# Optimization experiments

Hardware: AMD Instinct MI355X
Metric: run time of the kernel (lower is better)

The kernel has to match this reference:

```python
import jax, jax.numpy as jnp
import numpy as np

FS = 250; WIN = 250; STRIDE = 50; NC = 5; DM = 128; NH = 4; NL = 3; C = 62; L = 2000
BANDS = [(1, 4), (4, 8), (8, 12), (12, 16), (16, 20), (20, 30), (30, 45)]
UPDATE_RATE = 0.2
SIZES = np.array([13, 13, 12, 12, 12])  # channels//NC with remainder spread (62 = 2*13 + 3*12)
EPS = 1e-9


def _cdist(a, b):
    # Euclidean pairwise distance over last dim; ... batch dims broadcast.
    d2 = (a * a).sum(-1)[..., :, None] + (b * b).sum(-1)[..., None, :] \
         - 2.0 * jnp.einsum('...id,...jd->...ij', a, b)
    return jnp.sqrt(jnp.maximum(d2, 0.0))


def _extract_features(x):
    # PSDDEFeatureExtractor: sliding windows, hann, rfft, band power, DE, per-(b,c) normalization.
    b, c, l = x.shape
    nw = (l - WIN) // STRIDE + 1
    idx = np.arange(nw)[:, None] * STRIDE + np.arange(WIN)[None, :]
    win = x[:, :, idx]
    hann = 0.5 * (1.0 - jnp.cos(2.0 * jnp.pi * jnp.arange(WIN, dtype=x.dtype) / WIN))
    win = win * hann
    ps = jnp.abs(jnp.fft.rfft(win, n=WIN, axis=-1)) ** 2 / WIN  # (b,c,nw,126)
    psd = jnp.stack([ps[..., lo:hi].mean(-1) for lo, hi in BANDS], axis=-1)  # (b,c,nw,7)
    de = 0.5 * jnp.log(2.0 * jnp.pi * jnp.e * psd + EPS)
    def norm(f):
        m = f.mean((-2, -1), keepdims=True)
        s = f.std((-2, -1), keepdims=True, ddof=1)  # torch.std is unbiased
        return (f - m) / (s + EPS)
    return jnp.concatenate([norm(psd), norm(de)], axis=-1)     # (b,c,nw,14)


def _fps(dist, k):
    # Batched farthest-point sampling on (b,c,c) distance matrices -> (b,k) indices.
    take = lambda i: jnp.take_along_axis(dist, i[:, None, None], axis=1)[:, 0]  # (b,c)
    start = jnp.argmax(dist.sum(-1), axis=-1)                  # (b,)
    def step(md, _):
        far = jnp.argmax(md, axis=-1)
        return jnp.minimum(md, take(far)), far
    _, rest = jax.lax.scan(step, take(start), None, length=k - 1)
    return jnp.concatenate([start[:, None], rest.T], axis=1)


def _cluster_assignments(features, pos_emb):
    # ClusterManager.forward on fresh buffers (initialize -> temp centers -> EMA -> capacity assign).
    features = jax.lax.stop_gradient(features)
    pos_emb = jax.lax.stop_gradient(pos_emb)
    b, c = features.shape[:2]
    pos = pos_emb[0]                                           # (c,3)
    centers = pos[_fps(_cdist(pos, pos)[None], NC)[0]]         # (NC,3) FPS init
    # per-sample farthest channels on flattened features
    ff = features.reshape(b, c, -1)
    temp_idx = _fps(_cdist(ff, ff), NC)                        # (b,NC)
    center_coords = jnp.take_along_axis(pos_emb, temp_idx[:, :, None], axis=1)  # (b,NC,3)
    temp_assign = jnp.argmin(_cdist(pos_emb, center_coords), axis=-1)           # (b,c)
    flat_a = temp_assign.reshape(-1)
    flat_p = pos_emb.reshape(-1, 3)
    sums = jax.ops.segment_sum(flat_p, flat_a, num_segments=NC)
    cnts = jax.ops.segment_sum(jnp.ones((b * c,), flat_p.dtype), flat_a, num_segments=NC)
    avg = jnp.where(cnts[:, None] > 0, sums / jnp.maximum(cnts, 1.0)[:, None], 0.0)  # (NC,3)
    matching = jnp.argmin(_cdist(centers, avg), axis=1)
    centers = (1.0 - UPDATE_RATE) * centers + UPDATE_RATE * avg[matching]
    # capacity-constrained greedy assignment (sequential over channels)
    sizes = jnp.asarray(SIZES)
    order = jnp.argsort(_cdist(pos, centers), axis=1)          # (c,NC) preference order
    def step(counts, cand):
        avail = counts[cand] < sizes[cand]
        cl = cand[jnp.argmax(avail)]
        return counts.at[cl].add(1), cl
    _, assign = jax.lax.scan(step, jnp.zeros((NC,), jnp.int32), order)
    return assign                                              # (c,)


def _ln(x, g, b):
    m = x.mean(-1, keepdims=True)
    v = x.var(-1, keepdims=True)
    return (x - m) / jnp.sqrt(v + 1e-5) * g + b


def _mha(h, wqkv, bq, wo, bo_):
    b, t, d = h.shape
    dh = d // NH
    qkv = h @ wqkv.T + bq
    q, k, v = jnp.split(qkv, 3, axis=-1)
    sp = lambda z: z.reshape(b, t, NH, dh).transpose(0, 2, 1, 3)  # bhtd
    q, k, v = sp(q), sp(k), sp(v)
    att = jax.nn.softmax(jnp.einsum('bhqd,bhkd->bhqk', q, k) / jnp.sqrt(jnp.float32(dh)), axis=-1)
    o = jnp.einsum('bhqk,bhkd->bhqd', att, v).transpose(0, 2, 1, 3).reshape(b, t, d)
    return o @ wo.T + bo_


def _forward(x, pos_emb, proj_w, proj_b, proj_ln_g, proj_ln_b, pos_enc,
             Wqkv, bqkv, Wo, bo, W1, b1, W2, b2, ln1_g, ln1_b, ln2_g, ln2_b):
    b = x.shape[0]
    feats = _extract_features(x)                               # (b,C,36,14)
    pf = feats.reshape(b, C, -1) @ proj_w.T + proj_b
    pf = jax.nn.relu(_ln(pf, proj_ln_g, proj_ln_b))            # (b,C,DM)
    assign = _cluster_assignments(feats, pos_emb)              # (C,)
    # per-cluster mean of projected channel features (counts == SIZES by capacity constraint)
    sums = jax.ops.segment_sum(pf.swapaxes(0, 1), assign, num_segments=NC)  # (NC,b,DM)
    tokens = (sums / jnp.asarray(SIZES, pf.dtype)[:, None, None]).swapaxes(0, 1)  # (b,NC,DM)
    h = tokens + pos_enc
    for i in range(NL):  # post-norm TransformerEncoderLayer, eval mode (dropout=0)
        h = _ln(h + _mha(h, Wqkv[i], bqkv[i], Wo[i], bo[i]), ln1_g[i], ln1_b[i])
        ff = jax.nn.relu(h @ W1[i].T + b1[i]) @ W2[i].T + b2[i]
        h = _ln(h + ff, ln2_g[i], ln2_b[i])
    return h                                                   # (b,NC,DM)


def setup_inputs() -> dict:
    key = jax.random.key(0)
    ks = jax.random.split(key, 16)
    d_flat = 36 * 14  # n_windows * (7 psd + 7 de)
    s = 0.05
    return {
        'x': jax.random.normal(ks[0], (128, C, L), jnp.float32),
        'pos_emb': jax.random.normal(ks[1], (128, C, 3), jnp.float32),
        'proj_w': jax.random.normal(ks[2], (DM, d_flat), jnp.float32) * s,
        'proj_b': jax.random.normal(ks[3], (DM,), jnp.float32) * s,
        'proj_ln_g': jnp.ones((DM,), jnp.float32),
        'proj_ln_b': jnp.zeros((DM,), jnp.float32),
        'pos_enc': jax.random.normal(ks[4], (1, NC, DM), jnp.float32),
        'Wqkv': jax.random.normal(ks[5], (NL, 3 * DM, DM), jnp.float32) * s,
        'bqkv': jax.random.normal(ks[6], (NL, 3 * DM), jnp.float32) * s,
        'Wo': jax.random.normal(ks[7], (NL, DM, DM), jnp.float32) * s,
        'bo': jax.random.normal(ks[8], (NL, DM), jnp.float32) * s,
        'W1': jax.random.normal(ks[9], (NL, 2 * DM, DM), jnp.float32) * s,
        'b1': jax.random.normal(ks[10], (NL, 2 * DM), jnp.float32) * s,
        'W2': jax.random.normal(ks[11], (NL, DM, 2 * DM), jnp.float32) * s,
        'b2': jax.random.normal(ks[12], (NL, DM), jnp.float32) * s,
        'ln1_g': jnp.ones((NL, DM), jnp.float32),
        'ln1_b': jnp.zeros((NL, DM), jnp.float32),
        'ln2_g': jnp.ones((NL, DM), jnp.float32),
        'ln2_b': jnp.zeros((NL, DM), jnp.float32),
    }


def reference(x, pos_emb, proj_w, proj_b, proj_ln_g, proj_ln_b, pos_enc,
              Wqkv, bqkv, Wo, bo, W1, b1, W2, b2, ln1_g, ln1_b, ln2_g, ln2_b):
    return _forward(x, pos_emb, proj_w, proj_b, proj_ln_g, proj_ln_b, pos_enc,
                    Wqkv, bqkv, Wo, bo, W1, b1, W2, b2, ln1_g, ln1_b, ln2_g, ln2_b)
```

## Files before the change

### kernel.cpp

```cpp
#include <hip/hip_runtime.h>
#include <hip/hip_bf16.h>


typedef unsigned int u32;

#define N_SIG   7936
#define FDIM    504
#define DM      128

__device__ __constant__ int   bstart_c[7] = {1,4,8,12,16,20,30};
__device__ __constant__ int   bcnt_c[7]   = {3,4,4,4,4,10,15};
__device__ __constant__ float bandcnt_c[7] = {3.f,4.f,4.f,4.f,4.f,10.f,15.f};

__device__ __constant__ float twr_c[5] = {
    1.0f, 0.30901699437494745f, -0.8090169943749475f,
    -0.8090169943749475f, 0.30901699437494745f};
__device__ __constant__ float twi_c[5] = {
    0.0f, -0.9510565162951535f, -0.5877852522924731f,
    0.5877852522924731f, 0.9510565162951535f};

static __device__ __forceinline__ void bred2(float& a, float& b, volatile float* scr, int tid){
    #pragma unroll
    for (int off = 32; off > 0; off >>= 1){
        a += __shfl_down(a, off, 64);
        b += __shfl_down(b, off, 64);
    }
    if ((tid & 63) == 0){ scr[tid>>6] = a; scr[2 + (tid>>6)] = b; }
    __syncthreads();
    a = scr[0] + scr[1];
    b = scr[2] + scr[3];
    __syncthreads();
}

static __device__ __forceinline__ void bred2h(float& a, float& b, volatile float* scr, int tid){
    #pragma unroll
    for (int off = 32; off > 0; off >>= 1){
        a += __shfl_down(a, off, 64);
        b += __shfl_down(b, off, 64);
    }
    if (tid < 128 && (tid & 63) == 0){ scr[tid>>6] = a; scr[2 + (tid>>6)] = b; }
    __syncthreads();
    a = scr[0] + scr[1];
    b = scr[2] + scr[3];
    __syncthreads();
}

static __device__ __forceinline__ float2 combine5(const float* __restrict__ Cb,
                                                  int w, int kk){
    const int k5 = kk % 5;
    const float* cb = Cb + ((size_t)(w*46 + kk))*2;
    float ar = 0.f, ai = 0.f;
    int m = 0;
    #pragma unroll
    for (int c = 0; c < 5; ++c){
        float2 cv = *(const float2*)(cb + c*92);
        float tr = twr_c[m], ti = twi_c[m];
        ar = fmaf(tr, cv.x, ar); ar = fmaf(-ti, cv.y, ar);
        ai = fmaf(tr, cv.y, ai); ai = fmaf(ti, cv.x, ai);
        m += k5; if (m >= 5) m -= 5;
    }
    float2 o; o.x = ar; o.y = ai;
    return o;
}

__global__ __launch_bounds__(256) void basis_kernel(float* __restrict__ basis)
{
    int idx = blockIdx.x*256 + threadIdx.x;
    if (idx >= 1150) return;
    int kp = idx / 50;
    int n  = idx - kp*50;
    const float TPO = 0.025132741228718345f;
    int k0 = 2*kp, k1 = 2*kp + 1;
    float s0, c0, s1, c1;
    sincosf((float)((k0*n) % 250) * TPO, &s0, &c0);
    sincosf((float)((k1*n) % 250) * TPO, &s1, &c1);
    float4 v; v.x = c0; v.y = -s0; v.z = c1; v.w = -s1;
    ((float4*)basis)[idx] = v;
}

__global__ __launch_bounds__(256) void feat_kernel(
        const float* __restrict__ x, const float* __restrict__ basis,
        float* __restrict__ feats)
{
    __shared__ __align__(16) float xs[2000];
    __shared__ __align__(16) float Cb[3680];
    __shared__ float scr[16];

    const int tid = threadIdx.x;
    const int sig = blockIdx.x;

    {
        const float4* xg = (const float4*)(x + (size_t)sig*2000);
        for (int i = tid; i < 500; i += 256) ((float4*)xs)[i] = xg[i];
    }
    __syncthreads();

    for (int item = tid; item < 920; item += 256){
        const int kp = item / 40;
        const int j  = item - kp*40;
        const float2* xp = (const float2*)(xs + 50*j);
        const float4* bp = ((const float4*)basis) + kp*50;
        float cr0=0.f, ci0=0.f, cr1=0.f, ci1=0.f;
        #pragma unroll 5
        for (int t = 0; t < 25; ++t){
            float2 xv = xp[t];
            float4 b0 = bp[2*t], b1 = bp[2*t+1];
            cr0 = fmaf(xv.x, b0.x, cr0); ci0 = fmaf(xv.x, b0.y, ci0);
            cr1 = fmaf(xv.x, b0.z, cr1); ci1 = fmaf(xv.x, b0.w, ci1);
            cr0 = fmaf(xv.y, b1.x, cr0); ci0 = fmaf(xv.y, b1.y, ci0);
            cr1 = fmaf(xv.y, b1.z, cr1); ci1 = fmaf(xv.y, b1.w, ci1);
        }
        float4 o; o.x = cr0; o.y = ci0; o.z = cr1; o.w = ci1;
        *(float4*)(Cb + ((size_t)(j*46 + 2*kp))*2) = o;
    }
    __syncthreads();

    {
        const int i0 = tid, i1 = tid + 256, i2 = tid + 512, i3 = tid + 768;
        float2 r0, r1, r2, r3;
        { int w = 18 + i0/46, k = i0 - (i0/46)*46; r0 = combine5(Cb, w, k); }
        { int w = 18 + i1/46, k = i1 - (i1/46)*46; r1 = combine5(Cb, w, k); }
        { int w = 18 + i2/46, k = i2 - (i2/46)*46; r2 = combine5(Cb, w, k); }
        if (i3 < 828){ int w = 18 + i3/46, k = i3 - (i3/46)*46; r3 = combine5(Cb, w, k); }
        __syncthreads();
        { int w = 18 + i0/46, k = i0 - (i0/46)*46; *(float2*)(Cb + (w+4)*92 + 2*k) = r0; }
        { int w = 18 + i1/46, k = i1 - (i1/46)*46; *(float2*)(Cb + (w+4)*92 + 2*k) = r1; }
        { int w = 18 + i2/46, k = i2 - (i2/46)*46; *(float2*)(Cb + (w+4)*92 + 2*k) = r2; }
        if (i3 < 828){ int w = 18 + i3/46, k = i3 - (i3/46)*46; *(float2*)(Cb + (w+4)*92 + 2*k) = r3; }
    }
    __syncthreads();

    {
        const int i0 = tid, i1 = tid + 256, i2 = tid + 512, i3 = tid + 768;
        float2 r0, r1, r2, r3;
        { int w = i0/46, k = i0 - (i0/46)*46; r0 = combine5(Cb, w, k); }
        { int w = i1/46, k = i1 - (i1/46)*46; r1 = combine5(Cb, w, k); }
        { int w = i2/46, k = i2 - (i2/46)*46; r2 = combine5(Cb, w, k); }
        if (i3 < 828){ int w = i3/46, k = i3 - (i3/46)*46; r3 = combine5(Cb, w, k); }
        __syncthreads();
        { int w = i0/46, k = i0 - (i0/46)*46; *(float2*)(Cb + w*92 + 2*k) = r0; }
        { int w = i1/46, k = i1 - (i1/46)*46; *(float2*)(Cb + w*92 + 2*k) = r1; }
        { int w = i2/46, k = i2 - (i2/46)*46; *(float2*)(Cb + w*92 + 2*k) = r2; }
        if (i3 < 828){ int w = i3/46, k = i3 - (i3/46)*46; *(float2*)(Cb + w*92 + 2*k) = r3; }
    }
    __syncthreads();

    float psd = 0.f, de = 0.f;
    float s1p = 0.f, s2p = 0.f, s1d = 0.f, s2d = 0.f;
    int w = 0, bi = 0;
    if (tid < 252){
        w  = tid / 7;
        bi = tid - w*7;
        const int st = bstart_c[bi], cn = bcnt_c[bi];
        const float2* Xrow = (const float2*)(Cb + ((w < 18) ? w*92 : (w+4)*92));
        float2 xm = Xrow[st-1], xc = Xrow[st];
        float p = 0.f;
        for (int q = 0; q < cn; ++q){
            float2 xp = Xrow[st+q+1];
            float Hr = 0.5f*xc.x - 0.25f*(xm.x + xp.x);
            float Hi = 0.5f*xc.y - 0.25f*(xm.y + xp.y);
            p = fmaf(Hr, Hr, p); p = fmaf(Hi, Hi, p);
            xm = xc; xc = xp;
        }
        psd = p * (1.0f/250.0f) / bandcnt_c[bi];
        de  = 0.5f * logf(17.079468445347134f*psd + 1e-9f);
        s1p = psd; s2p = psd*psd; s1d = de; s2d = de*de;
    }
    #pragma unroll
    for (int off = 32; off > 0; off >>= 1){
        s1p += __shfl_down(s1p, off, 64); s2p += __shfl_down(s2p, off, 64);
        s1d += __shfl_down(s1d, off, 64); s2d += __shfl_down(s2d, off, 64);
    }
    {
        const int wid = tid >> 6;
        if ((tid & 63) == 0){
            scr[0*4 + wid] = s1p; scr[1*4 + wid] = s2p;
            scr[2*4 + wid] = s1d; scr[3*4 + wid] = s2d;
        }
    }
    __syncthreads();
    s1p = scr[0] + scr[1] + scr[2]  + scr[3];
    s2p = scr[4] + scr[5] + scr[6]  + scr[7];
    s1d = scr[8] + scr[9] + scr[10] + scr[11];
    s2d = scr[12] + scr[13] + scr[14] + scr[15];

    if (tid < 252){
        float mp = s1p / 252.f;
        float vp = fmaxf((s2p - 252.f*mp*mp) / 251.f, 0.f);
        float sp = sqrtf(vp) + 1e-9f;
        float md = s1d / 252.f;
        float vd = fmaxf((s2d - 252.f*md*md) / 251.f, 0.f);
        float sd = sqrtf(vd) + 1e-9f;
        float* ob = feats + (size_t)sig * FDIM;
        ob[w*14 + bi]     = (psd - mp) / sp;
        ob[w*14 + 7 + bi] = (de  - md) / sd;
    }
}

__global__ __launch_bounds__(512) void dist_kernel(
        const float* __restrict__ feats, float* __restrict__ dmg)
{
    __shared__ float Fc[62*130];

    const int tid = threadIdx.x;
    const int b   = blockIdx.x >> 1;
    const int h   = blockIdx.x & 1;
    const int nt  = h ? 465 : 496;

    int ti = 0, tj = 0;
    const bool act = tid < nt;
    if (act){ ti = (h ? 16 : 0) + tid/31; tj = tid - (tid/31)*31; }

    float a00 = 0.f, a01 = 0.f, a10 = 0.f, a11 = 0.f;

    for (int ch = 0; ch < 4; ++ch){
        if (ch) __syncthreads();
        for (int i = tid; i < 62*63; i += 512){
            int r = i / 63, dc2 = i - r*63;
            *(float2*)(Fc + r*130 + 2*dc2) =
                *(const float2*)(feats + ((size_t)b*62 + r)*FDIM + ch*126 + 2*dc2);
        }
        __syncthreads();
        if (act){
            const float2* ri0 = (const float2*)(Fc + (2*ti)*130);
            const float2* ri1 = (const float2*)(Fc + (2*ti+1)*130);
            const float2* rj0 = (const float2*)(Fc + (2*tj)*130);
            const float2* rj1 = (const float2*)(Fc + (2*tj+1)*130);
            for (int g = 0; g < 9; ++g){
                const int q0 = g*7;
                float2 A0[7], A1[7], C0[7], C1[7];
                #pragma unroll
                for (int u = 0; u < 7; ++u){
                    A0[u] = ri0[q0+u]; A1[u] = ri1[q0+u];
                    C0[u] = rj0[q0+u]; C1[u] = rj1[q0+u];
                }
                #pragma unroll
                for (int u = 0; u < 7; ++u){
                    float d;
                    d = A0[u].x-C0[u].x; a00 = fmaf(d,d,a00); d = A0[u].y-C0[u].y; a00 = fmaf(d,d,a00);
                    d = A0[u].x-C1[u].x; a01 = fmaf(d,d,a01); d = A0[u].y-C1[u].y; a01 = fmaf(d,d,a01);
                    d = A1[u].x-C0[u].x; a10 = fmaf(d,d,a10); d = A1[u].y-C0[u].y; a10 = fmaf(d,d,a10);
                    d = A1[u].x-C1[u].x; a11 = fmaf(d,d,a11); d = A1[u].y-C1[u].y; a11 = fmaf(d,d,a11);
                }
            }
        }
    }
    if (act){
        float* dst = dmg + (size_t)b*3844;
        dst[(2*ti)*62   + 2*tj]   = sqrtf(a00);
        dst[(2*ti)*62   + 2*tj+1] = sqrtf(a01);
        dst[(2*ti+1)*62 + 2*tj]   = sqrtf(a10);
        dst[(2*ti+1)*62 + 2*tj+1] = sqrtf(a11);
    }
}

__global__ __launch_bounds__(64) void fps_kernel(
        const float* __restrict__ dmg, const float* __restrict__ pos_emb,
        float* __restrict__ pbuf)
{
    __shared__ float Dm[3844];
    __shared__ float mdv[62];
    __shared__ float rsv[62];
    __shared__ int   seli[5];
    __shared__ float ccen[5][3];
    __shared__ int   sbest[62];
    __shared__ float sp3[62][3];

    const int tid = threadIdx.x;
    const int b   = blockIdx.x;

    {
        const float4* src = (const float4*)(dmg + (size_t)b*3844);
        for (int i = tid; i < 961; i += 64) ((float4*)Dm)[i] = src[i];
    }
    __syncthreads();

    if (tid < 62){ float s = 0.f; for (int j = 0; j < 62; ++j) s += Dm[tid*62 + j]; rsv[tid] = s; }
    __syncthreads();
    if (tid == 0){
        int bi = 0; float bv = rsv[0];
        for (int i = 1; i < 62; ++i) if (rsv[i] > bv){ bv = rsv[i]; bi = i; }
        seli[0] = bi;
    }
    __syncthreads();
    if (tid < 62) mdv[tid] = Dm[seli[0]*62 + tid];
    __syncthreads();
    for (int it = 1; it < 5; ++it){
        if (tid == 0){
            int bi = 0; float bv = mdv[0];
            for (int i = 1; i < 62; ++i) if (mdv[i] > bv){ bv = mdv[i]; bi = i; }
            seli[it] = bi;
        }
        __syncthreads();
        if (tid < 62) mdv[tid] = fminf(mdv[tid], Dm[seli[it]*62 + tid]);
        __syncthreads();
    }
    if (tid < 5){
        int c0 = seli[tid];
        #pragma unroll
        for (int j = 0; j < 3; ++j) ccen[tid][j] = pos_emb[((size_t)b*62 + c0)*3 + j];
    }
    __syncthreads();
    if (tid < 62){
        float px = pos_emb[((size_t)b*62 + tid)*3 + 0];
        float py = pos_emb[((size_t)b*62 + tid)*3 + 1];
        float pz = pos_emb[((size_t)b*62 + tid)*3 + 2];
        int best = 0; float bd = 3.4e38f;
        #pragma unroll
        for (int t = 0; t < 5; ++t){
            float dx = px - ccen[t][0], dy = py - ccen[t][1], dz = pz - ccen[t][2];
            float d2 = dx*dx + dy*dy + dz*dz;
            if (d2 < bd){ bd = d2; best = t; }
        }
        sbest[tid] = best;
        sp3[tid][0] = px; sp3[tid][1] = py; sp3[tid][2] = pz;
    }
    __syncthreads();
    if (tid < 5){
        float sx = 0.f, sy = 0.f, sz = 0.f, cnt = 0.f;
        for (int c = 0; c < 62; ++c){
            if (sbest[c] == tid){
                sx += sp3[c][0]; sy += sp3[c][1]; sz += sp3[c][2]; cnt += 1.f;
            }
        }
        float* dst = pbuf + (size_t)b*20;
        dst[tid*3 + 0] = sx; dst[tid*3 + 1] = sy; dst[tid*3 + 2] = sz;
        dst[15 + tid]  = cnt;
    }
}

__global__ __launch_bounds__(64) void finalize_kernel(
        const float* __restrict__ pos_emb, const float* __restrict__ pbuf,
        int* __restrict__ assign_out)
{
    __shared__ float P[62*3];
    __shared__ float Dp[62*62];
    __shared__ float rsv[62];
    __shared__ float mdv[62];
    __shared__ int   seli[5];
    __shared__ float cenS[5][3];
    __shared__ int   ordS[62][5];
    __shared__ float gs[15];
    __shared__ float gc[5];
    const int tid = threadIdx.x;

    if (tid < 20){
        float s = 0.f;
        for (int b = 0; b < 128; ++b) s += pbuf[(size_t)b*20 + tid];
        if (tid < 15) gs[tid] = s; else gc[tid-15] = s;
    }
    if (tid < 62){
        #pragma unroll
        for (int j = 0; j < 3; ++j) P[tid*3 + j] = pos_emb[(size_t)tid*3 + j];
    }
    __syncthreads();
    if (tid < 62){
        float xi = P[tid*3], yi = P[tid*3+1], zi = P[tid*3+2];
        float s = 0.f;
        for (int j = 0; j < 62; ++j){
            float dx = xi - P[j*3], dy = yi - P[j*3+1], dz = zi - P[j*3+2];
            float d = sqrtf(dx*dx + dy*dy + dz*dz);
            Dp[tid*62 + j] = d; s += d;
        }
        rsv[tid] = s;
    }
    __syncthreads();
    if (tid == 0){
        int bi = 0; float bv = rsv[0];
        for (int i = 1; i < 62; ++i) if (rsv[i] > bv){ bv = rsv[i]; bi = i; }
        seli[0] = bi;
        for (int i = 0; i < 62; ++i) mdv[i] = Dp[bi*62 + i];
        for (int it = 1; it < 5; ++it){
            int fi = 0; float fv = mdv[0];
            for (int i = 1; i < 62; ++i) if (mdv[i] > fv){ fv = mdv[i]; fi = i; }
            seli[it] = fi;
            for (int i = 0; i < 62; ++i) mdv[i] = fminf(mdv[i], Dp[fi*62 + i]);
        }
        float cen[5][3], avg[5][3];
        for (int t = 0; t < 5; ++t)
            for (int j = 0; j < 3; ++j) cen[t][j] = P[seli[t]*3 + j];
        for (int t = 0; t < 5; ++t){
            float c = gc[t];
            for (int j = 0; j < 3; ++j)
                avg[t][j] = (c > 0.f) ? gs[t*3 + j] / fmaxf(c, 1.f) : 0.f;
        }
        for (int i = 0; i < 5; ++i){
            int m = 0; float bv2 = 3.4e38f;
            for (int j = 0; j < 5; ++j){
                float dx = cen[i][0]-avg[j][0], dy = cen[i][1]-avg[j][1], dz = cen[i][2]-avg[j][2];
                float d2 = dx*dx + dy*dy + dz*dz;
                if (d2 < bv2){ bv2 = d2; m = j; }
            }
            for (int j = 0; j < 3; ++j) cenS[i][j] = 0.8f*cen[i][j] + 0.2f*avg[m][j];
        }
    }
    __syncthreads();
    if (tid < 62){
        float dd[5];
        #pragma unroll
        for (int t = 0; t < 5; ++t){
            float dx = P[tid*3]-cenS[t][0], dy = P[tid*3+1]-cenS[t][1], dz = P[tid*3+2]-cenS[t][2];
            dd[t] = sqrtf(dx*dx + dy*dy + dz*dz);
        }
        bool tk[5] = {false,false,false,false,false};
        #pragma unroll
        for (int s = 0; s < 5; ++s){
            int best = -1;
            #pragma unroll
            for (int t = 0; t < 5; ++t)
                if (!tk[t] && (best < 0 || dd[t] < dd[best])) best = t;
            tk[best] = true; ordS[tid][s] = best;
        }
    }
    __syncthreads();
    if (tid == 0){
        const int sizesA[5] = {13,13,12,12,12};
        int counts[5] = {0,0,0,0,0};
        for (int i = 0; i < 62; ++i){
            int cl = ordS[i][0];
            #pragma unroll
            for (int s = 0; s < 5; ++s){
                int t = ordS[i][s];
                if (counts[t] < sizesA[t]){ cl = t; break; }
            }
            counts[cl]++;
            assign_out[i] = cl;
        }
    }
}

__global__ __launch_bounds__(128) void proj_kernel(
        const float* __restrict__ feats, const float* __restrict__ proj_w,
        const float* __restrict__ proj_b, const float* __restrict__ lng,
        const float* __restrict__ lnb, float* __restrict__ pf)
{
    __shared__ float fs[8*FDIM];
    __shared__ float scr[4];
    const int tid = threadIdx.x;
    const int row0 = blockIdx.x * 8;

    for (int i = tid; i < 8*FDIM; i += 128)
        fs[i] = feats[(size_t)row0*FDIM + i];
    __syncthreads();

    const int dg = tid >> 2;
    const int rp = tid & 3;

    float acc[4][2];
    #pragma unroll
    for (int dd = 0; dd < 4; ++dd){
        float bb = proj_b[dg*4 + dd];
        acc[dd][0] = bb; acc[dd][1] = bb;
    }

    const float4* w0 = (const float4*)(proj_w + (size_t)(dg*4+0)*FDIM);
    const float4* w1 = (const float4*)(proj_w + (size_t)(dg*4+1)*FDIM);
    const float4* w2 = (const float4*)(proj_w + (size_t)(dg*4+2)*FDIM);
    const float4* w3 = (const float4*)(proj_w + (size_t)(dg*4+3)*FDIM);
    const float4* f0 = (const float4*)(fs + (rp*2+0)*FDIM);
    const float4* f1 = (const float4*)(fs + (rp*2+1)*FDIM);

    for (int kc = 0; kc < 63; ++kc){
        float4 p0 = f0[2*kc], q0 = f0[2*kc+1];
        float4 p1 = f1[2*kc], q1 = f1[2*kc+1];
        const float4* wd[4] = {w0, w1, w2, w3};
        #pragma unroll
        for (int dd = 0; dd < 4; ++dd){
            float4 wA = wd[dd][2*kc], wB = wd[dd][2*kc+1];
            float s = acc[dd][0];
            s = fmaf(p0.x,wA.x,s); s = fmaf(p0.y,wA.y,s); s = fmaf(p0.z,wA.z,s); s = fmaf(p0.w,wA.w,s);
            s = fmaf(q0.x,wB.x,s); s = fmaf(q0.y,wB.y,s); s = fmaf(q0.z,wB.z,s); s = fmaf(q0.w,wB.w,s);
            acc[dd][0] = s;
            s = acc[dd][1];
            s = fmaf(p1.x,wA.x,s); s = fmaf(p1.y,wA.y,s); s = fmaf(p1.z,wA.z,s); s = fmaf(p1.w,wA.w,s);
            s = fmaf(q1.x,wB.x,s); s = fmaf(q1.y,wB.y,s); s = fmaf(q1.z,wB.z,s); s = fmaf(q1.w,wB.w,s);
            acc[dd][1] = s;
        }
    }
    __syncthreads();

    #pragma unroll
    for (int dd = 0; dd < 4; ++dd){
        fs[(rp*2+0)*128 + dg*4 + dd] = acc[dd][0];
        fs[(rp*2+1)*128 + dg*4 + dd] = acc[dd][1];
    }
    __syncthreads();

    const float gl = lng[tid], bl = lnb[tid];
    #pragma unroll
    for (int g = 0; g < 8; ++g){
        float v = fs[g*128 + tid];
        float s1 = v, s2 = v*v;
        bred2(s1, s2, scr, tid);
        float m = s1 * (1.f/128.f);
        float var = fmaxf(s2 * (1.f/128.f) - m*m, 0.f);
        float y = (v - m) / sqrtf(var + 1e-5f);
        y = y*gl + bl;
        pf[(size_t)(row0 + g)*DM + tid] = fmaxf(y, 0.f);
    }
}

__global__ __launch_bounds__(256) void former_kernel(
        const float* __restrict__ pf, const int* __restrict__ assign,
        const float* __restrict__ pos_enc,
        const float* __restrict__ Wqkv, const float* __restrict__ bqkv,
        const float* __restrict__ Wo,   const float* __restrict__ bo,
        const float* __restrict__ W1,   const float* __restrict__ b1,
        const float* __restrict__ W2,   const float* __restrict__ b2,
        const float* __restrict__ ln1g, const float* __restrict__ ln1b,
        const float* __restrict__ ln2g, const float* __restrict__ ln2b,
        float* __restrict__ out)
{
    __shared__ float h[5*128];
    __shared__ float qkvL[5*384];
    __shared__ float attL[100];
    __shared__ float oL[5*128];
    __shared__ float hidL[5*256];
    __shared__ int   asg[62];
    __shared__ float scr[4];

    const int b   = blockIdx.x;
    const int tid = threadIdx.x;
    const int d   = tid & 127;
    const int kh  = tid >> 7;

    if (tid < 62) asg[tid] = assign[tid];
    __syncthreads();

    if (kh == 0){
        float a0=0,a1=0,a2=0,a3=0,a4=0;
        const float* pfb = pf + (size_t)b*62*DM + d;
        for (int c = 0; c < 62; ++c){
            float v = pfb[(size_t)c*DM];
            int a = asg[c];
            a0 += (a==0)?v:0.f; a1 += (a==1)?v:0.f; a2 += (a==2)?v:0.f;
            a3 += (a==3)?v:0.f; a4 += (a==4)?v:0.f;
        }
        h[0*128+d] = a0/13.f + pos_enc[0*128+d];
        h[1*128+d] = a1/13.f + pos_enc[1*128+d];
        h[2*128+d] = a2/12.f + pos_enc[2*128+d];
        h[3*128+d] = a3/12.f + pos_enc[3*128+d];
        h[4*128+d] = a4/12.f + pos_enc[4*128+d];
    }
    __syncthreads();

    for (int L = 0; L < 3; ++L){
        const float* Wq = Wqkv + (size_t)L*384*128;
        {
            float acc[3][5];
            #pragma unroll
            for (int rr = 0; rr < 3; ++rr){
                float bb = (kh == 0) ? bqkv[L*384 + rr*128 + d] : 0.f;
                #pragma unroll
                for (int t = 0; t < 5; ++t) acc[rr][t] = bb;
            }
            for (int kc = kh*8; kc < kh*8 + 8; ++kc){
                float hr[5][8];
                #pragma unroll
                for (int t = 0; t < 5; ++t){
                    float4 p = *(const float4*)&h[t*128 + kc*8];
                    float4 q = *(const float4*)&h[t*128 + kc*8 + 4];
                    hr[t][0]=p.x; hr[t][1]=p.y; hr[t][2]=p.z; hr[t][3]=p.w;
                    hr[t][4]=q.x; hr[t][5]=q.y; hr[t][6]=q.z; hr[t][7]=q.w;
                }
                #pragma unroll
                for (int rr = 0; rr < 3; ++rr){
                    float4 wA = *(const float4*)(Wq + ((size_t)(rr*128 + d))*128 + kc*8);
                    float4 wB = *(const float4*)(Wq + ((size_t)(rr*128 + d))*128 + kc*8 + 4);
                    #pragma unroll
                    for (int t = 0; t < 5; ++t){
                        float s = acc[rr][t];
                        s=fmaf(hr[t][0],wA.x,s); s=fmaf(hr[t][1],wA.y,s);
                        s=fmaf(hr[t][2],wA.z,s); s=fmaf(hr[t][3],wA.w,s);
                        s=fmaf(hr[t][4],wB.x,s); s=fmaf(hr[t][5],wB.y,s);
                        s=fmaf(hr[t][6],wB.z,s); s=fmaf(hr[t][7],wB.w,s);
                        acc[rr][t] = s;
                    }
                }
            }
            if (kh == 1){
                #pragma unroll
                for (int rr = 0; rr < 3; ++rr)
                    #pragma unroll
                    for (int t = 0; t < 5; ++t)
                        qkvL[t*384 + rr*128 + d] = acc[rr][t];
            }
            __syncthreads();
            if (kh == 0){
                #pragma unroll
                for (int rr = 0; rr < 3; ++rr)
                    #pragma unroll
                    for (int t = 0; t < 5; ++t)
                        qkvL[t*384 + rr*128 + d] = acc[rr][t] + qkvL[t*384 + rr*128 + d];
            }
            __syncthreads();
        }

        if (tid < 100){
            int hh = tid/25, rem = tid - hh*25, tq = rem/5, tk = rem - (rem/5)*5;
            const float* qq = &qkvL[tq*384 + hh*32];
            const float* kk = &qkvL[tk*384 + 128 + hh*32];
            float s = 0.f;
            #pragma unroll
            for (int j = 0; j < 32; ++j) s = fmaf(qq[j], kk[j], s);
            attL[tid] = s * 0.17677669529663687f;
        }
        __syncthreads();
        if (tid < 20){
            int hh = tid/5, tq = tid - hh*5;
            float* row = &attL[hh*25 + tq*5];
            float mx = row[0];
            #pragma unroll
            for (int j = 1; j < 5; ++j) mx = fmaxf(mx, row[j]);
            float sm = 0.f;
            #pragma unroll
            for (int j = 0; j < 5; ++j){ float e = expf(row[j]-mx); row[j] = e; sm += e; }
            float inv = 1.f/sm;
            #pragma unroll
            for (int j = 0; j < 5; ++j) row[j] *= inv;
        }
        __syncthreads();

        {
            int hh = d >> 5;
            int t0 = kh ? 3 : 0, t1 = kh ? 5 : 3;
            for (int t = t0; t < t1; ++t){
                float s = 0.f;
                #pragma unroll
                for (int tk = 0; tk < 5; ++tk)
                    s = fmaf(attL[hh*25 + t*5 + tk], qkvL[tk*384 + 256 + d], s);
                oL[t*128 + d] = s;
            }
        }
        __syncthreads();

        float val[5];
        {
            float bv = (kh == 0) ? bo[L*128 + d] : 0.f;
            #pragma unroll
            for (int t = 0; t < 5; ++t) val[t] = bv;
            const float* WoR = Wo + ((size_t)L*128 + d)*128;
            for (int kc = kh*8; kc < kh*8 + 8; ++kc){
                float orr[5][8];
                #pragma unroll
                for (int t = 0; t < 5; ++t){
                    float4 p = *(const float4*)&oL[t*128 + kc*8];
                    float4 q = *(const float4*)&oL[t*128 + kc*8 + 4];
                    orr[t][0]=p.x; orr[t][1]=p.y; orr[t][2]=p.z; orr[t][3]=p.w;
                    orr[t][4]=q.x; orr[t][5]=q.y; orr[t][6]=q.z; orr[t][7]=q.w;
                }
                float4 wA = *(const float4*)(WoR + kc*8);
                float4 wB = *(const float4*)(WoR + kc*8 + 4);
                #pragma unroll
                for (int t = 0; t < 5; ++t){
                    float s = val[t];
                    s=fmaf(orr[t][0],wA.x,s); s=fmaf(orr[t][1],wA.y,s);
                    s=fmaf(orr[t][2],wA.z,s); s=fmaf(orr[t][3],wA.w,s);
                    s=fmaf(orr[t][4],wB.x,s); s=fmaf(orr[t][5],wB.y,s);
                    s=fmaf(orr[t][6],wB.z,s); s=fmaf(orr[t][7],wB.w,s);
                    val[t] = s;
                }
            }
            if (kh == 1){
                #pragma unroll
                for (int t = 0; t < 5; ++t) hidL[t*128 + d] = val[t];
            }
            __syncthreads();
            if (kh == 0){
                #pragma unroll
                for (int t = 0; t < 5; ++t)
                    val[t] = (val[t] + hidL[t*128 + d]) + h[t*128 + d];
            }
            __syncthreads();
        }
        {
            float ng = ln1g[L*128 + d], nb = ln1b[L*128 + d];
            #pragma unroll
            for (int t = 0; t < 5; ++t){
                float s1 = val[t], s2 = val[t]*val[t];
                bred2h(s1, s2, scr, tid);
                float m = s1*(1.f/128.f);
                float var = fmaxf(s2*(1.f/128.f) - m*m, 0.f);
                float y = (val[t] - m) / sqrtf(var + 1e-5f);
                if (kh == 0) h[t*128 + d] = y*ng + nb;
            }
        }
        __syncthreads();

        {
            float f1[2][5];
            #pragma unroll
            for (int rr = 0; rr < 2; ++rr){
                float bb = (kh == 0) ? b1[L*256 + rr*128 + d] : 0.f;
                #pragma unroll
                for (int t = 0; t < 5; ++t) f1[rr][t] = bb;
            }
            const float* W1b = W1 + (size_t)L*256*128;
            for (int kc = kh*8; kc < kh*8 + 8; ++kc){
                float hr[5][8];
                #pragma unroll
                for (int t = 0; t < 5; ++t){
                    float4 p = *(const float4*)&h[t*128 + kc*8];
                    float4 q = *(const float4*)&h[t*128 + kc*8 + 4];
                    hr[t][0]=p.x; hr[t][1]=p.y; hr[t][2]=p.z; hr[t][3]=p.w;
                    hr[t][4]=q.x; hr[t][5]=q.y; hr[t][6]=q.z; hr[t][7]=q.w;
                }
                #pragma unroll
                for (int rr = 0; rr < 2; ++rr){
                    float4 wA = *(const float4*)(W1b + ((size_t)(rr*128 + d))*128 + kc*8);
                    float4 wB = *(const float4*)(W1b + ((size_t)(rr*128 + d))*128 + kc*8 + 4);
                    #pragma unroll
                    for (int t = 0; t < 5; ++t){
                        float s = f1[rr][t];
                        s=fmaf(hr[t][0],wA.x,s); s=fmaf(hr[t][1],wA.y,s);
                        s=fmaf(hr[t][2],wA.z,s); s=fmaf(hr[t][3],wA.w,s);
                        s=fmaf(hr[t][4],wB.x,s); s=fmaf(hr[t][5],wB.y,s);
                        s=fmaf(hr[t][6],wB.z,s); s=fmaf(hr[t][7],wB.w,s);
                        f1[rr][t] = s;
                    }
                }
            }
            if (kh == 1){
                #pragma unroll
                for (int rr = 0; rr < 2; ++rr)
                    #pragma unroll
                    for (int t = 0; t < 5; ++t)
                        qkvL[rr*640 + t*128 + d] = f1[rr][t];
            }
            __syncthreads();
            if (kh == 0){
                #pragma unroll
                for (int rr = 0; rr < 2; ++rr)
                    #pragma unroll
                    for (int t = 0; t < 5; ++t)
                        hidL[t*256 + rr*128 + d] =
                            fmaxf(f1[rr][t] + qkvL[rr*640 + t*128 + d], 0.f);
            }
            __syncthreads();
        }

        {
            float v2[5];
            float bv = (kh == 0) ? b2[L*128 + d] : 0.f;
            #pragma unroll
            for (int t = 0; t < 5; ++t) v2[t] = bv;
            const float* W2R = W2 + ((size_t)L*128 + d)*256;
            for (int kc = kh*16; kc < kh*16 + 16; ++kc){
                float hr[5][8];
                #pragma unroll
                for (int t = 0; t < 5; ++t){
                    float4 p = *(const float4*)&hidL[t*256 + kc*8];
                    float4 q = *(const float4*)&hidL[t*256 + kc*8 + 4];
                    hr[t][0]=p.x; hr[t][1]=p.y; hr[t][2]=p.z; hr[t][3]=p.w;
                    hr[t][4]=q.x; hr[t][5]=q.y; hr[t][6]=q.z; hr[t][7]=q.w;
                }
                float4 wA = *(const float4*)(W2R + kc*8);
                float4 wB = *(const float4*)(W2R + kc*8 + 4);
                #pragma unroll
                for (int t = 0; t < 5; ++t){
                    float s = v2[t];
                    s=fmaf(hr[t][0],wA.x,s); s=fmaf(hr[t][1],wA.y,s);
                    s=fmaf(hr[t][2],wA.z,s); s=fmaf(hr[t][3],wA.w,s);
                    s=fmaf(hr[t][4],wB.x,s); s=fmaf(hr[t][5],wB.y,s);
                    s=fmaf(hr[t][6],wB.z,s); s=fmaf(hr[t][7],wB.w,s);
                    v2[t] = s;
                }
            }
            if (kh == 1){
                #pragma unroll
                for (int t = 0; t < 5; ++t) qkvL[t*128 + d] = v2[t];
            }
            __syncthreads();
            if (kh == 0){
                #pragma unroll
                for (int t = 0; t < 5; ++t)
                    v2[t] = (v2[t] + qkvL[t*128 + d]) + h[t*128 + d];
            }
            __syncthreads();
            float ng = ln2g[L*128 + d], nb = ln2b[L*128 + d];
            #pragma unroll
            for (int t = 0; t < 5; ++t){
                float s1 = v2[t], s2 = v2[t]*v2[t];
                bred2h(s1, s2, scr, tid);
                float m = s1*(1.f/128.f);
                float var = fmaxf(s2*(1.f/128.f) - m*m, 0.f);
                float y = (v2[t] - m) / sqrtf(var + 1e-5f);
                if (kh == 0) h[t*128 + d] = y*ng + nb;
            }
        }
        __syncthreads();
    }

    if (kh == 0){
        #pragma unroll
        for (int t = 0; t < 5; ++t)
            out[((size_t)b*5 + t)*128 + d] = h[t*128 + d];
    }
}

extern "C" void kernel_launch(void* const* d_in, const int* in_sizes, int n_in,
                              void* d_out, int out_size, void* d_ws, size_t ws_size,
                              hipStream_t stream)
{
    const float* x        = (const float*)d_in[0];
    const float* pos_emb  = (const float*)d_in[1];
    const float* proj_w   = (const float*)d_in[2];
    const float* proj_b   = (const float*)d_in[3];
    const float* proj_lng = (const float*)d_in[4];
    const float* proj_lnb = (const float*)d_in[5];
    const float* pos_enc  = (const float*)d_in[6];
    const float* Wqkv     = (const float*)d_in[7];
    const float* bqkv     = (const float*)d_in[8];
    const float* Wo       = (const float*)d_in[9];
    const float* bo       = (const float*)d_in[10];
    const float* W1       = (const float*)d_in[11];
    const float* b1       = (const float*)d_in[12];
    const float* W2       = (const float*)d_in[13];
    const float* b2       = (const float*)d_in[14];
    const float* ln1g     = (const float*)d_in[15];
    const float* ln1b     = (const float*)d_in[16];
    const float* ln2g     = (const float*)d_in[17];
    const float* ln2b     = (const float*)d_in[18];

    float* ws    = (float*)d_ws;
    float* feats = ws;
    float* pf    = feats + (size_t)N_SIG*FDIM;
    float* gsums = pf + (size_t)N_SIG*DM;
    float* gcnt  = gsums + 15;
    int*   assign = (int*)(gcnt + 5);
    float* basis = (float*)(assign + 64);
    float* pbuf  = basis + 4600;
    float* dmg   = pf;

    float* out = (float*)d_out;

    basis_kernel<<<5, 256, 0, stream>>>(basis);
    feat_kernel<<<N_SIG, 256, 0, stream>>>(x, basis, feats);
    dist_kernel<<<256, 512, 0, stream>>>(feats, dmg);
    fps_kernel<<<128, 64, 0, stream>>>(dmg, pos_emb, pbuf);
    finalize_kernel<<<1, 64, 0, stream>>>(pos_emb, pbuf, assign);
    proj_kernel<<<992, 128, 0, stream>>>(feats, proj_w, proj_b, proj_lng, proj_lnb, pf);
    former_kernel<<<128, 256, 0, stream>>>(pf, assign, pos_enc,
        Wqkv, bqkv, Wo, bo, W1, b1, W2, b2, ln1g, ln1b, ln2g, ln2b, out);
}
```

Measured before the change: 520.1 us.

## Split transformer matmuls four ways across 512 threads and merge FFT combine stages

The former kernel grows from 256 to 512 threads per block. Each projection's K dimension is split four ways, and three partial sums are reduced through a new shared-memory buffer; the attention-output loop is redistributed to match. In the feature kernel, the two radix-5 combine stages are merged so one barrier goes away, and combine5 loads all five inputs before doing the FMAs. The aim is more parallelism in the 128-block transformer kernel, at the cost of extra shared memory, partial-sum traffic and fewer registers per thread.

```diff
diff --git a/kernel.cpp b/kernel.cpp
--- a/kernel.cpp
+++ b/kernel.cpp
@@ -49,14 +49,16 @@
                                                   int w, int kk){
     const int k5 = kk % 5;
     const float* cb = Cb + ((size_t)(w*46 + kk))*2;
+    float2 cv[5];
+    #pragma unroll
+    for (int c = 0; c < 5; ++c) cv[c] = *(const float2*)(cb + c*92);
     float ar = 0.f, ai = 0.f;
     int m = 0;
     #pragma unroll
     for (int c = 0; c < 5; ++c){
-        float2 cv = *(const float2*)(cb + c*92);
         float tr = twr_c[m], ti = twi_c[m];
-        ar = fmaf(tr, cv.x, ar); ar = fmaf(-ti, cv.y, ar);
-        ai = fmaf(tr, cv.y, ai); ai = fmaf(ti, cv.x, ai);
+        ar = fmaf(tr, cv[c].x, ar); ar = fmaf(-ti, cv[c].y, ar);
+        ai = fmaf(tr, cv[c].y, ai); ai = fmaf(ti, cv[c].x, ai);
         m += k5; if (m >= 5) m -= 5;
     }
     float2 o; o.x = ar; o.y = ai;
@@ -127,21 +129,16 @@
         { int w = 18 + i1/46, k = i1 - (i1/46)*46; *(float2*)(Cb + (w+4)*92 + 2*k) = r1; }
         { int w = 18 + i2/46, k = i2 - (i2/46)*46; *(float2*)(Cb + (w+4)*92 + 2*k) = r2; }
         if (i3 < 828){ int w = 18 + i3/46, k = i3 - (i3/46)*46; *(float2*)(Cb + (w+4)*92 + 2*k) = r3; }
-    }
-    __syncthreads();
-
-    {
-        const int i0 = tid, i1 = tid + 256, i2 = tid + 512, i3 = tid + 768;
-        float2 r0, r1, r2, r3;
-        { int w = i0/46, k = i0 - (i0/46)*46; r0 = combine5(Cb, w, k); }
-        { int w = i1/46, k = i1 - (i1/46)*46; r1 = combine5(Cb, w, k); }
-        { int w = i2/46, k = i2 - (i2/46)*46; r2 = combine5(Cb, w, k); }
-        if (i3 < 828){ int w = i3/46, k = i3 - (i3/46)*46; r3 = combine5(Cb, w, k); }
-        __syncthreads();
-        { int w = i0/46, k = i0 - (i0/46)*46; *(float2*)(Cb + w*92 + 2*k) = r0; }
-        { int w = i1/46, k = i1 - (i1/46)*46; *(float2*)(Cb + w*92 + 2*k) = r1; }
-        { int w = i2/46, k = i2 - (i2/46)*46; *(float2*)(Cb + w*92 + 2*k) = r2; }
-        if (i3 < 828){ int w = i3/46, k = i3 - (i3/46)*46; *(float2*)(Cb + w*92 + 2*k) = r3; }
+        float2 s0, s1, s2, s3;
+        { int w = i0/46, k = i0 - (i0/46)*46; s0 = combine5(Cb, w, k); }
+        { int w = i1/46, k = i1 - (i1/46)*46; s1 = combine5(Cb, w, k); }
+        { int w = i2/46, k = i2 - (i2/46)*46; s2 = combine5(Cb, w, k); }
+        if (i3 < 828){ int w = i3/46, k = i3 - (i3/46)*46; s3 = combine5(Cb, w, k); }
+        __syncthreads();
+        { int w = i0/46, k = i0 - (i0/46)*46; *(float2*)(Cb + w*92 + 2*k) = s0; }
+        { int w = i1/46, k = i1 - (i1/46)*46; *(float2*)(Cb + w*92 + 2*k) = s1; }
+        { int w = i2/46, k = i2 - (i2/46)*46; *(float2*)(Cb + w*92 + 2*k) = s2; }
+        if (i3 < 828){ int w = i3/46, k = i3 - (i3/46)*46; *(float2*)(Cb + w*92 + 2*k) = s3; }
     }
     __syncthreads();
 
@@ -500,7 +497,7 @@
     }
 }
 
-__global__ __launch_bounds__(256) void former_kernel(
+__global__ __launch_bounds__(512) void former_kernel(
         const float* __restrict__ pf, const int* __restrict__ assign,
         const float* __restrict__ pos_enc,
         const float* __restrict__ Wqkv, const float* __restrict__ bqkv,
@@ -516,18 +513,19 @@
     __shared__ float attL[100];
     __shared__ float oL[5*128];
     __shared__ float hidL[5*256];
+    __shared__ float part[3*1920];
     __shared__ int   asg[62];
     __shared__ float scr[4];
 
     const int b   = blockIdx.x;
     const int tid = threadIdx.x;
     const int d   = tid & 127;
-    const int kh  = tid >> 7;
+    const int kq  = tid >> 7;
 
     if (tid < 62) asg[tid] = assign[tid];
     __syncthreads();
 
-    if (kh == 0){
+    if (kq == 0){
         float a0=0,a1=0,a2=0,a3=0,a4=0;
         const float* pfb = pf + (size_t)b*62*DM + d;
         for (int c = 0; c < 62; ++c){
@@ -550,11 +548,11 @@
             float acc[3][5];
             #pragma unroll
             for (int rr = 0; rr < 3; ++rr){
-                float bb = (kh == 0) ? bqkv[L*384 + rr*128 + d] : 0.f;
+                float bb = (kq == 0) ? bqkv[L*384 + rr*128 + d] : 0.f;
                 #pragma unroll
                 for (int t = 0; t < 5; ++t) acc[rr][t] = bb;
             }
-            for (int kc = kh*8; kc < kh*8 + 8; ++kc){
+            for (int kc = kq*4; kc < kq*4 + 4; ++kc){
                 float hr[5][8];
                 #pragma unroll
                 for (int t = 0; t < 5; ++t){
@@ -578,20 +576,22 @@
                     }
                 }
             }
-            if (kh == 1){
+            if (kq > 0){
                 #pragma unroll
                 for (int rr = 0; rr < 3; ++rr)
                     #pragma unroll
                     for (int t = 0; t < 5; ++t)
-                        qkvL[t*384 + rr*128 + d] = acc[rr][t];
+                        part[(kq-1)*1920 + t*384 + rr*128 + d] = acc[rr][t];
             }
             __syncthreads();
-            if (kh == 0){
+            if (kq == 0){
                 #pragma unroll
                 for (int rr = 0; rr < 3; ++rr)
                     #pragma unroll
-                    for (int t = 0; t < 5; ++t)
-                        qkvL[t*384 + rr*128 + d] = acc[rr][t] + qkvL[t*384 + rr*128 + d];
+                    for (int t = 0; t < 5; ++t){
+                        int o = t*384 + rr*128 + d;
+                        qkvL[o] = ((acc[rr][t] + part[o]) + part[1920 + o]) + part[3840 + o];
+                    }
             }
             __syncthreads();
         }
@@ -623,24 +623,31 @@
 
         {
             int hh = d >> 5;
-            int t0 = kh ? 3 : 0, t1 = kh ? 5 : 3;
-            for (int t = t0; t < t1; ++t){
+            int tA = kq;
+            {
                 float s = 0.f;
                 #pragma unroll
                 for (int tk = 0; tk < 5; ++tk)
-                    s = fmaf(attL[hh*25 + t*5 + tk], qkvL[tk*384 + 256 + d], s);
-                oL[t*128 + d] = s;
+                    s = fmaf(attL[hh*25 + tA*5 + tk], qkvL[tk*384 + 256 + d], s);
+                oL[tA*128 + d] = s;
+            }
+            if (kq == 0){
+                float s = 0.f;
+                #pragma unroll
+                for (int tk = 0; tk < 5; ++tk)
+                    s = fmaf(attL[hh*25 + 4*5 + tk], qkvL[tk*384 + 256 + d], s);
+                oL[4*128 + d] = s;
             }
         }
         __syncthreads();
 
         float val[5];
         {
-            float bv = (kh == 0) ? bo[L*128 + d] : 0.f;
+            float bv = (kq == 0) ? bo[L*128 + d] : 0.f;
             #pragma unroll
             for (int t = 0; t < 5; ++t) val[t] = bv;
             const float* WoR = Wo + ((size_t)L*128 + d)*128;
-            for (int kc = kh*8; kc < kh*8 + 8; ++kc){
+            for (int kc = kq*4; kc < kq*4 + 4; ++kc){
                 float orr[5][8];
                 #pragma unroll
                 for (int t = 0; t < 5; ++t){
@@ -661,15 +668,19 @@
                     val[t] = s;
                 }
             }
-            if (kh == 1){
-                #pragma unroll
-                for (int t = 0; t < 5; ++t) hidL[t*128 + d] = val[t];
+            if (kq > 0){
+                #pragma unroll
+                for (int t = 0; t < 5; ++t)
+                    part[(kq-1)*1920 + t*128 + d] = val[t];
             }
             __syncthreads();
-            if (kh == 0){
-                #pragma unroll
-                for (int t = 0; t < 5; ++t)
-                    val[t] = (val[t] + hidL[t*128 + d]) + h[t*128 + d];
+            if (kq == 0){
+                #pragma unroll
+                for (int t = 0; t < 5; ++t){
+                    int o = t*128 + d;
+                    val[t] = (((val[t] + part[o]) + part[1920 + o]) + part[3840 + o])
+                             + h[t*128 + d];
+                }
             }
             __syncthreads();
         }
@@ -682,7 +693,7 @@
                 float m = s1*(1.f/128.f);
                 float var = fmaxf(s2*(1.f/128.f) - m*m, 0.f);
                 float y = (val[t] - m) / sqrtf(var + 1e-5f);
-                if (kh == 0) h[t*128 + d] = y*ng + nb;
+                if (kq == 0) h[t*128 + d] = y*ng + nb;
             }
         }
         __syncthreads();
@@ -691,12 +702,12 @@
             float f1[2][5];
             #pragma unroll
             for (int rr = 0; rr < 2; ++rr){
-                float bb = (kh == 0) ? b1[L*256 + rr*128 + d] : 0.f;
+                float bb = (kq == 0) ? b1[L*256 + rr*128 + d] : 0.f;
                 #pragma unroll
                 for (int t = 0; t < 5; ++t) f1[rr][t] = bb;
             }
             const float* W1b = W1 + (size_t)L*256*128;
-            for (int kc = kh*8; kc < kh*8 + 8; ++kc){
+            for (int kc = kq*4; kc < kq*4 + 4; ++kc){
                 float hr[5][8];
                 #pragma unroll
                 for (int t = 0; t < 5; ++t){
@@ -720,32 +731,34 @@
                     }
                 }
             }
-            if (kh == 1){
+            if (kq > 0){
                 #pragma unroll
                 for (int rr = 0; rr < 2; ++rr)
                     #pragma unroll
                     for (int t = 0; t < 5; ++t)
-                        qkvL[rr*640 + t*128 + d] = f1[rr][t];
+                        part[(kq-1)*1920 + rr*640 + t*128 + d] = f1[rr][t];
             }
             __syncthreads();
-            if (kh == 0){
+            if (kq == 0){
                 #pragma unroll
                 for (int rr = 0; rr < 2; ++rr)
                     #pragma unroll
-                    for (int t = 0; t < 5; ++t)
-                        hidL[t*256 + rr*128 + d] =
-                            fmaxf(f1[rr][t] + qkvL[rr*640 + t*128 + d], 0.f);
+                    for (int t = 0; t < 5; ++t){
+                        int o = rr*640 + t*128 + d;
+                        float v = ((f1[rr][t] + part[o]) + part[1920 + o]) + part[3840 + o];
+                        hidL[t*256 + rr*128 + d] = fmaxf(v, 0.f);
+                    }
             }
             __syncthreads();
         }
 
         {
             float v2[5];
-            float bv = (kh == 0) ? b2[L*128 + d] : 0.f;
+            float bv = (kq == 0) ? b2[L*128 + d] : 0.f;
             #pragma unroll
             for (int t = 0; t < 5; ++t) v2[t] = bv;
             const float* W2R = W2 + ((size_t)L*128 + d)*256;
-            for (int kc = kh*16; kc < kh*16 + 16; ++kc){
+            for (int kc = kq*8; kc < kq*8 + 8; ++kc){
                 float hr[5][8];
                 #pragma unroll
                 for (int t = 0; t < 5; ++t){
@@ -766,15 +779,18 @@
                     v2[t] = s;
                 }
             }
-            if (kh == 1){
-                #pragma unroll
-                for (int t = 0; t < 5; ++t) qkvL[t*128 + d] = v2[t];
+            if (kq > 0){
+                #pragma unroll
+                for (int t = 0; t < 5; ++t) part[(kq-1)*1920 + t*128 + d] = v2[t];
             }
             __syncthreads();
-            if (kh == 0){
-                #pragma unroll
-                for (int t = 0; t < 5; ++t)
-                    v2[t] = (v2[t] + qkvL[t*128 + d]) + h[t*128 + d];
+            if (kq == 0){
+                #pragma unroll
+                for (int t = 0; t < 5; ++t){
+                    int o = t*128 + d;
+                    v2[t] = (((v2[t] + part[o]) + part[1920 + o]) + part[3840 + o])
+                            + h[t*128 + d];
+                }
             }
             __syncthreads();
             float ng = ln2g[L*128 + d], nb = ln2b[L*128 + d];
@@ -785,13 +801,13 @@
                 float m = s1*(1.f/128.f);
                 float var = fmaxf(s2*(1.f/128.f) - m*m, 0.f);
                 float y = (v2[t] - m) / sqrtf(var + 1e-5f);
-                if (kh == 0) h[t*128 + d] = y*ng + nb;
-            }
-        }
-        __syncthreads();
-    }
-
-    if (kh == 0){
+                if (kq == 0) h[t*128 + d] = y*ng + nb;
+            }
+        }
+        __syncthreads();
+    }
+
+    if (kq == 0){
         #pragma unroll
         for (int t = 0; t < 5; ++t)
             out[((size_t)b*5 + t)*128 + d] = h[t*128 + d];
@@ -840,6 +856,6 @@
     fps_kernel<<<128, 64, 0, stream>>>(dmg, pos_emb, pbuf);
     finalize_kernel<<<1, 64, 0, stream>>>(pos_emb, pbuf, assign);
     proj_kernel<<<992, 128, 0, stream>>>(feats, proj_w, proj_b, proj_lng, proj_lnb, pf);
-    former_kernel<<<128, 256, 0, stream>>>(pf, assign, pos_enc,
+    former_kernel<<<128, 512, 0, stream>>>(pf, assign, pos_enc,
         Wqkv, bqkv, Wo, bo, W1, b1, W2, b2, ln1g, ln1b, ln2g, ln2b, out);
 }
```

Result: no change. 518.5 us (-0.3%).
